# Optimization experiments

Measured on AMD Instinct MI355X. Metric: run time of the kernel, lower is better.

Reference implementation:

```python
import jax, jax.numpy as jnp
import numpy as np

NUM_BINS = 11
SIGMA = 0.1
EMB = 110
FC2 = 512
NUM_CLASSES = 4
DN = ('NCHW', 'OIHW', 'NCHW')


def conv(x, w, b, stride, pad):
    y = jax.lax.conv_general_dilated(x, w, (stride, stride), [(pad, pad), (pad, pad)], dimension_numbers=DN)
    return y + b[None, :, None, None]


def conv_transpose(x, w, b, stride):
    # torch ConvTranspose2d(k=3, padding=1, output_padding=stride-1)
    # == dilated conv with flipped, channel-swapped kernel
    wf = jnp.flip(w, (2, 3)).transpose(1, 0, 2, 3)  # (Cin,Cout,kh,kw)->(Cout,Cin,kh,kw)
    pad = (1, 1 + stride - 1)  # (k-1-p, k-1-p+output_padding)
    y = jax.lax.conv_general_dilated(x, wf, (1, 1), [pad, pad], lhs_dilation=(stride, stride), dimension_numbers=DN)
    return y + b[None, :, None, None]


def kde(data, num_bins, bandwidth):
    # data: (B, N, F) -> (B, F*num_bins), vectorized over features
    pts = jnp.linspace(0.0, 1.0, num_bins, dtype=data.dtype)  # (bins,)
    c = 1.0 / (bandwidth * np.sqrt(2.0 * np.pi))
    coef = -1.0 / (2.0 * bandwidth ** 2)
    diff2 = (pts[None, None, None, :] - data[..., None]) ** 2  # (B,N,F,bins)
    gk = c * jnp.exp(coef * diff2)
    dens = gk.sum(axis=1)  # (B,F,bins) -- integrate over instances
    dens = dens / dens.sum(axis=2, keepdims=True)
    B = data.shape[0]
    return dens.reshape(B, -1)  # feature-major concat, same as torch cat over features


def setup_inputs() -> dict:
    key = jax.random.key(0)
    ks = jax.random.split(key, 16)
    B, N = 64, 32
    g = lambda k, shape, s=0.05: (jax.random.normal(k, shape, dtype=jnp.float32) * s)
    inp = {
        'x': jax.random.uniform(ks[0], (B, N, 3, 32, 32), dtype=jnp.float32),
        'ew1': g(ks[1], (16, 3, 3, 3)), 'eb1': jnp.full((16,), 0.1, jnp.float32),
        'ew2': g(ks[2], (32, 16, 3, 3)), 'eb2': jnp.full((32,), 0.1, jnp.float32),
        'ew3': g(ks[3], (64, 32, 3, 3)), 'eb3': jnp.full((64,), 0.1, jnp.float32),
        'kw': g(ks[4], (EMB, 64 * 8 * 8), 0.02), 'kb': jnp.zeros((EMB,), jnp.float32),
        'dw1': g(ks[5], (64, 64, 3, 3)), 'db1': jnp.zeros((64,), jnp.float32),
        'dw2': g(ks[6], (64, 32, 3, 3)), 'db2': jnp.zeros((32,), jnp.float32),
        'dw3': g(ks[7], (32, 16, 3, 3)), 'db3': jnp.zeros((16,), jnp.float32),
        'dw4': g(ks[8], (3, 16, 1, 1)), 'db4': jnp.full((3,), 0.1, jnp.float32),
        'f1w': g(ks[9], (FC2, EMB * NUM_BINS), 0.02), 'f1b': jnp.zeros((FC2,), jnp.float32),
        'f2w': g(ks[10], (FC2 // 2, FC2), 0.02), 'f2b': jnp.zeros((FC2 // 2,), jnp.float32),
        'f3w': g(ks[11], (NUM_CLASSES, FC2 // 2), 0.02), 'f3b': jnp.zeros((NUM_CLASSES,), jnp.float32),
    }
    return inp


def reference(x, ew1, eb1, ew2, eb2, ew3, eb3, kw, kb,
              dw1, db1, dw2, db2, dw3, db3, dw4, db4,
              f1w, f1b, f2w, f2b, f3w, f3b):
    B, N, C, H, W = x.shape
    xf = x.reshape(B * N, C, H, W)
    # encoder
    h = jax.nn.relu(conv(xf, ew1, eb1, 1, 1))   # (BN,16,32,32)
    h = jax.nn.relu(conv(h, ew2, eb2, 2, 1))    # (BN,32,16,16)
    h = jax.nn.relu(conv(h, ew3, eb3, 2, 1))    # (BN,64,8,8)
    # decoder
    d = jax.nn.relu(conv_transpose(h, dw1, db1, 2))  # (BN,64,16,16)
    d = jax.nn.relu(conv_transpose(d, dw2, db2, 2))  # (BN,32,32,32)
    d = jax.nn.relu(conv_transpose(d, dw3, db3, 1))  # (BN,16,32,32)
    d = conv(d, dw4, db4, 1, 0)                      # (BN,3,32,32)
    decoded_img = d.reshape(B, N, C, H, W)
    # KDE embeddings
    emb = jax.nn.sigmoid(h.reshape(B * N, -1) @ kw.T + kb)  # (BN,EMB)
    emb = emb.reshape(B, N, EMB)
    fd = kde(emb, NUM_BINS, SIGMA)  # (B, EMB*NUM_BINS)
    # MLP classifier (dropout p=0 -> identity)
    m = jax.nn.relu(fd @ f1w.T + f1b)
    m = jax.nn.relu(m @ f2w.T + f2b)
    logits = m @ f3w.T + f3b
    return (logits, decoded_img)
```

## Files before the change

### kernel.cpp

```cpp
#include <hip/hip_runtime.h>
#include <hip/hip_bf16.h>
#include <stdint.h>

typedef __hip_bfloat16 bf16;
typedef __attribute__((ext_vector_type(8))) short short8;
typedef __attribute__((ext_vector_type(4))) float f32x4;

__device__ __forceinline__ bf16 f2b(float v){ return __float2bfloat16(v); }
__device__ __forceinline__ short s2s(float v){ bf16 b = __float2bfloat16(v); return *reinterpret_cast<short*>(&b); }
__device__ __forceinline__ short8 s8zero()
{
    short8 z;
    for (int i = 0; i < 8; ++i) z[i] = 0;
    return z;
}

__global__ void prep_weights(const float* __restrict__ ew1, const float* __restrict__ ew2,
                             const float* __restrict__ ew3, const float* __restrict__ dw1,
                             const float* __restrict__ dw2, const float* __restrict__ dw3,
                             const float* __restrict__ kw,  const float* __restrict__ f1w,
                             const float* __restrict__ f2w,
                             bf16* __restrict__ wte1, bf16* __restrict__ wte2,
                             bf16* __restrict__ wte3, bf16* __restrict__ wtb4,
                             bf16* __restrict__ wtb5, bf16* __restrict__ wtb6,
                             bf16* __restrict__ kwt,  bf16* __restrict__ wtf1,
                             bf16* __restrict__ wtf2)
{
    int idx = blockIdx.x * blockDim.x + threadIdx.x;
    if (idx < 1536) {
        int q = idx >> 9, r = idx & 511;
        int co = r >> 5, k = r & 31;
        int j = k >> 3, ci = k & 7;
        int t = 4 * q + j;
        float v = (ci < 3 && t < 9) ? ew1[((size_t)co * 3 + ci) * 9 + t] : 0.f;
        wte1[idx] = f2b(v);
        return;
    }
    idx -= 1536;
    if (idx < 5120) {
        int p = idx >> 10, r = idx & 1023;
        int co = r >> 5, k = r & 31;
        int t = 2 * p + (k >> 4);
        int ch = k & 15;
        float v = (t <= 8) ? ew2[((size_t)co * 16 + ch) * 9 + t] : 0.f;
        wte2[idx] = f2b(v);
        return;
    }
    idx -= 5120;
    if (idx < 18432) {
        int co = idx / 288;
        int r  = idx - co * 288;
        int ci = r / 9, t = r - ci * 9;
        wte3[((size_t)t * 64 + co) * 32 + ci] = f2b(ew3[idx]);
        return;
    }
    idx -= 18432;
    if (idx < 36864) {
        int ci = idx / 576;
        int r  = idx - ci * 576;
        int co = r / 9, t = r - co * 9;
        wtb4[((size_t)t * 64 + co) * 64 + ci] = f2b(dw1[idx]);
        return;
    }
    idx -= 36864;
    if (idx < 18432) {
        int ci = idx / 288;
        int r  = idx - ci * 288;
        int co = r / 9, t = r - co * 9;
        wtb5[((size_t)t * 32 + co) * 64 + ci] = f2b(dw2[idx]);
        return;
    }
    idx -= 18432;
    if (idx < 4608) {
        int ci = idx / 144;
        int r  = idx - ci * 144;
        int co = r / 9, t = r - co * 9;
        wtb6[((size_t)t * 16 + co) * 32 + ci] = f2b(dw3[idx]);
        return;
    }
    idx -= 4608;
    if (idx < 458752) {
        int e = idx >> 12, kk = idx & 4095;
        int pos = kk >> 6, ci = kk & 63;
        float v = (e < 110) ? kw[(size_t)e * 4096 + ci * 64 + pos] : 0.f;
        kwt[idx] = f2b(v);
        return;
    }
    idx -= 458752;
    if (idx < 655360) {
        int n = idx / 1280, k = idx - n * 1280;
        float v = (k < 1210) ? f1w[(size_t)n * 1210 + k] : 0.f;
        wtf1[idx] = f2b(v);
        return;
    }
    idx -= 655360;
    if (idx < 131072) {
        wtf2[idx] = f2b(f2w[idx]);
        return;
    }
}

__global__ __launch_bounds__(256)
void enc123_fused(const float* __restrict__ xg,
                  const bf16* __restrict__ wte1, const float* __restrict__ eb1,
                  const bf16* __restrict__ wte2, const float* __restrict__ eb2,
                  const bf16* __restrict__ wte3, const float* __restrict__ eb3,
                  bf16* __restrict__ h3g)
{
    __shared__ char smem[57728];
    short8* H1  = (short8*)smem;
    short8* Xs1 = (short8*)(smem + 36992);
    short8* H2  = (short8*)(smem + 36992);

    const int img = blockIdx.x;
    const int tid = threadIdx.x;
    const float* xi = xg + (size_t)img * 3072;

    for (int e = tid; e < 1156; e += 256) {
        int hr = e / 34, wc = e % 34;
        int hi = hr - 1, wi = wc - 1;
        short8 v = s8zero();
        if ((unsigned)hi < 32u && (unsigned)wi < 32u) {
            int p = hi * 32 + wi;
            v[0] = s2s(xi[p]);
            v[1] = s2s(xi[p + 1024]);
            v[2] = s2s(xi[p + 2048]);
        }
        Xs1[e] = v;
    }
    for (int e = tid; e < 264; e += 256) {
        int c8 = e & 1, q = e >> 1;
        int pl = q / 33, j = q % 33;
        int pos = (j < 17) ? j : (j - 16) * 17;
        H1[(pl * 289 + pos) * 2 + c8] = s8zero();
    }
    __syncthreads();

    const int wv = tid >> 6, lane = tid & 63;
    const int lp = lane & 15, lq = lane >> 4;

    {
        short8 wf[3];
        #pragma unroll
        for (int q = 0; q < 3; ++q)
            wf[q] = *reinterpret_cast<const short8*>(wte1 + (size_t)(q * 16 + lp) * 32 + lq * 8);
        float bv[4];
        #pragma unroll
        for (int r = 0; r < 4; ++r) bv[r] = eb1[lq * 4 + r];

        for (int mt = wv * 16; mt < wv * 16 + 16; ++mt) {
            int m = mt * 16 + lp;
            int ho = m >> 5, wo = m & 31;
            f32x4 acc = {0.f, 0.f, 0.f, 0.f};
            #pragma unroll
            for (int q = 0; q < 3; ++q) {
                int t = 4 * q + lq;
                if (t > 8) t = 8;
                int pos = (ho + t / 3) * 34 + (wo + t % 3);
                acc = __builtin_amdgcn_mfma_f32_16x16x32_bf16(wf[q], Xs1[pos], acc, 0, 0, 0);
            }
            int pl  = (ho & 1) * 2 + (wo & 1);
            int pos = ((ho >> 1) + 1) * 17 + ((wo >> 1) + 1);
            int slot = (pl * 289 + pos) * 2 + ((lq >> 1) ^ (pos & 1));
            __align__(8) bf16 ov[4];
            #pragma unroll
            for (int r = 0; r < 4; ++r) ov[r] = f2b(fmaxf(acc[r] + bv[r], 0.f));
            *reinterpret_cast<uint2*>(reinterpret_cast<char*>(&H1[slot]) + (lq & 1) * 8)
                = *reinterpret_cast<uint2*>(ov);
        }
    }
    __syncthreads();

    for (int e = tid; e < 272; e += 256) {
        int c8 = e & 3, q = e >> 2;
        int pl = q / 17, j = q % 17;
        int pos = (j < 9) ? j : (j - 8) * 9;
        H2[(pl * 81 + pos) * 4 + c8] = s8zero();
    }
    {
        const int nt = wv & 1, mh = wv >> 1;
        short8 wf[5];
        #pragma unroll
        for (int p = 0; p < 5; ++p)
            wf[p] = *reinterpret_cast<const short8*>(wte2 + ((size_t)(p * 32 + nt * 16 + lp)) * 32 + lq * 8);
        float bv[4];
        #pragma unroll
        for (int r = 0; r < 4; ++r) bv[r] = eb2[nt * 16 + lq * 4 + r];

        for (int mt = mh * 8; mt < mh * 8 + 8; ++mt) {
            int m = mt * 16 + lp;
            int ho = m >> 4, wo = m & 15;
            f32x4 acc = {0.f, 0.f, 0.f, 0.f};
            #pragma unroll
            for (int p = 0; p < 5; ++p) {
                const int tA = 2 * p, tB = (p < 4) ? 2 * p + 1 : 8;
                const int khA = tA / 3, kwA = tA % 3;
                const int paA = (khA == 1) ? 0 : 1, dhA = (khA == 0) ? -1 : 0;
                const int pbA = (kwA == 1) ? 0 : 1, dwA = (kwA == 0) ? -1 : 0;
                const int khB = tB / 3, kwB = tB % 3;
                const int paB = (khB == 1) ? 0 : 1, dhB = (khB == 0) ? -1 : 0;
                const int pbB = (kwB == 1) ? 0 : 1, dwB = (kwB == 0) ? -1 : 0;
                int posA = (ho + dhA + 1) * 17 + (wo + dwA + 1);
                int posB = (ho + dhB + 1) * 17 + (wo + dwB + 1);
                int idxA = ((paA * 2 + pbA) * 289 + posA) * 2 + ((lq & 1) ^ (posA & 1));
                int idxB = ((paB * 2 + pbB) * 289 + posB) * 2 + ((lq & 1) ^ (posB & 1));
                short8 b = H1[(lq < 2) ? idxA : idxB];
                acc = __builtin_amdgcn_mfma_f32_16x16x32_bf16(wf[p], b, acc, 0, 0, 0);
            }
            int pl  = (ho & 1) * 2 + (wo & 1);
            int pos = ((ho >> 1) + 1) * 9 + ((wo >> 1) + 1);
            int c8w = nt * 2 + (lq >> 1);
            int slot = (pl * 81 + pos) * 4 + (c8w ^ (pos & 3));
            __align__(8) bf16 ov[4];
            #pragma unroll
            for (int r = 0; r < 4; ++r) ov[r] = f2b(fmaxf(acc[r] + bv[r], 0.f));
            *reinterpret_cast<uint2*>(reinterpret_cast<char*>(&H2[slot]) + (lq & 1) * 8)
                = *reinterpret_cast<uint2*>(ov);
        }
    }
    __syncthreads();

    {
        const int nt = wv;
        short8 wf[9];
        #pragma unroll
        for (int t = 0; t < 9; ++t)
            wf[t] = *reinterpret_cast<const short8*>(wte3 + ((size_t)(t * 64 + nt * 16 + lp)) * 32 + lq * 8);
        float bv[4];
        #pragma unroll
        for (int r = 0; r < 4; ++r) bv[r] = eb3[nt * 16 + lq * 4 + r];

        bf16* yi = h3g + (size_t)img * 4096;
        for (int mt = 0; mt < 4; ++mt) {
            int m = mt * 16 + lp;
            int ho = m >> 3, wo = m & 7;
            f32x4 acc = {0.f, 0.f, 0.f, 0.f};
            #pragma unroll
            for (int t = 0; t < 9; ++t) {
                const int kh = t / 3, kw2 = t % 3;
                const int pa = (kh == 1) ? 0 : 1, dh = (kh == 0) ? -1 : 0;
                const int pb = (kw2 == 1) ? 0 : 1, dw = (kw2 == 0) ? -1 : 0;
                int pos = (ho + dh + 1) * 9 + (wo + dw + 1);
                int idx = ((pa * 2 + pb) * 81 + pos) * 4 + (lq ^ (pos & 3));
                acc = __builtin_amdgcn_mfma_f32_16x16x32_bf16(wf[t], H2[idx], acc, 0, 0, 0);
            }
            __align__(8) bf16 ov[4];
            #pragma unroll
            for (int r = 0; r < 4; ++r) ov[r] = f2b(fmaxf(acc[r] + bv[r], 0.f));
            *reinterpret_cast<uint2*>(yi + ((size_t)(ho * 8 + wo)) * 64 + nt * 16 + lq * 4)
                = *reinterpret_cast<uint2*>(ov);
        }
    }
}

__global__ __launch_bounds__(256)
void dec12_fused(const bf16* __restrict__ h3g,
                 const bf16* __restrict__ wtb4, const float* __restrict__ db1,
                 const bf16* __restrict__ wtb5, const float* __restrict__ db2,
                 bf16* __restrict__ d2p)
{
    __shared__ short8 H3s[648];
    __shared__ short8 D1s[2312];
    const int img = blockIdx.x;
    const int tid = threadIdx.x;
    const bf16* xi = h3g + (size_t)img * 4096;

    for (int e = tid; e < 648; e += 256) {
        int c8 = e & 7, pos = e >> 3;
        int hl = pos / 9, wi = pos % 9;
        short8 v = s8zero();
        if (hl < 8 && wi < 8)
            v = *reinterpret_cast<const short8*>(xi + ((size_t)(hl * 8 + wi)) * 64 + c8 * 8);
        H3s[pos * 8 + (c8 ^ (pos & 7))] = v;
    }
    for (int e = tid; e < 264; e += 256) {
        int c8 = e & 7, q = e >> 3;
        int pos = (q < 17) ? (16 * 17 + q) : ((q - 17) * 17 + 16);
        D1s[pos * 8 + c8] = s8zero();
    }
    __syncthreads();

    const int wv = tid >> 6, lane = tid & 63;
    const int lp = lane & 15, lq = lane >> 4;

    {
        const int nt = wv;
        short8 wf[9][2];
        #pragma unroll
        for (int t = 0; t < 9; ++t) {
            const bf16* wp = wtb4 + ((size_t)t * 64 + nt * 16 + lp) * 64 + lq * 8;
            wf[t][0] = *reinterpret_cast<const short8*>(wp);
            wf[t][1] = *reinterpret_cast<const short8*>(wp + 32);
        }
        float bv[4];
        #pragma unroll
        for (int r = 0; r < 4; ++r) bv[r] = db1[nt * 16 + lq * 4 + r];

        const int c8w = nt * 2 + (lq >> 1);
        for (int mt = 0; mt < 4; ++mt) {
            int m = mt * 16 + lp;
            int hq = m >> 3, wq = m & 7;
            f32x4 zero = {0.f, 0.f, 0.f, 0.f};
            f32x4 acc[4] = {zero, zero, zero, zero};
            #pragma unroll
            for (int kh = 0; kh < 3; ++kh) {
                #pragma unroll
                for (int kw = 0; kw < 3; ++kw) {
                    const int pa = (kh + 1) & 1, pb = (kw + 1) & 1;
                    const int oh = (pa + 1 - kh) >> 1, ow = (pb + 1 - kw) >> 1;
                    const int cls = pa * 2 + pb;
                    const int t = kh * 3 + kw;
                    int pos = (hq + oh) * 9 + (wq + ow);
                    int sw = pos & 7;
                    acc[cls] = __builtin_amdgcn_mfma_f32_16x16x32_bf16(wf[t][0], H3s[pos * 8 + (lq ^ sw)], acc[cls], 0, 0, 0);
                    acc[cls] = __builtin_amdgcn_mfma_f32_16x16x32_bf16(wf[t][1], H3s[pos * 8 + ((4 + lq) ^ sw)], acc[cls], 0, 0, 0);
                }
            }
            #pragma unroll
            for (int cls = 0; cls < 4; ++cls) {
                int pa = cls >> 1, pb = cls & 1;
                int ho = hq * 2 + pa, wo = wq * 2 + pb;
                int pos = ho * 17 + wo;
                int slot = pos * 8 + (c8w ^ (pos & 7));
                __align__(8) bf16 ov[4];
                #pragma unroll
                for (int r = 0; r < 4; ++r) ov[r] = f2b(fmaxf(acc[cls][r] + bv[r], 0.f));
                *reinterpret_cast<uint2*>(reinterpret_cast<char*>(&D1s[slot]) + (lq & 1) * 8)
                    = *reinterpret_cast<uint2*>(ov);
            }
        }
    }
    __syncthreads();

    {
        const int nt = wv & 1;
        const int mt0 = (wv >> 1) * 8;
        short8 wf[9][2];
        #pragma unroll
        for (int t = 0; t < 9; ++t) {
            const bf16* wp = wtb5 + ((size_t)t * 32 + nt * 16 + lp) * 64 + lq * 8;
            wf[t][0] = *reinterpret_cast<const short8*>(wp);
            wf[t][1] = *reinterpret_cast<const short8*>(wp + 32);
        }
        float bv[4];
        #pragma unroll
        for (int r = 0; r < 4; ++r) bv[r] = db2[nt * 16 + lq * 4 + r];

        bf16* yo = d2p + (size_t)img * 32768;
        for (int mt = mt0; mt < mt0 + 8; ++mt) {
            const int hq = mt, wq = lp;
            f32x4 zero = {0.f, 0.f, 0.f, 0.f};
            f32x4 acc[4] = {zero, zero, zero, zero};
            #pragma unroll
            for (int kh = 0; kh < 3; ++kh) {
                #pragma unroll
                for (int kw = 0; kw < 3; ++kw) {
                    const int pa = (kh + 1) & 1, pb = (kw + 1) & 1;
                    const int oh = (pa + 1 - kh) >> 1, ow = (pb + 1 - kw) >> 1;
                    const int cls = pa * 2 + pb;
                    const int t = kh * 3 + kw;
                    int pos = (hq + oh) * 17 + (wq + ow);
                    int sw = pos & 7;
                    acc[cls] = __builtin_amdgcn_mfma_f32_16x16x32_bf16(wf[t][0], D1s[pos * 8 + (lq ^ sw)], acc[cls], 0, 0, 0);
                    acc[cls] = __builtin_amdgcn_mfma_f32_16x16x32_bf16(wf[t][1], D1s[pos * 8 + ((4 + lq) ^ sw)], acc[cls], 0, 0, 0);
                }
            }
            #pragma unroll
            for (int cls = 0; cls < 4; ++cls) {
                __align__(8) bf16 ov[4];
                #pragma unroll
                for (int r = 0; r < 4; ++r) ov[r] = f2b(fmaxf(acc[cls][r] + bv[r], 0.f));
                size_t off = (size_t)cls * 8192 + (size_t)nt * 4096 + (hq * 16 + wq) * 16 + lq * 4;
                *reinterpret_cast<uint2*>(yo + off) = *reinterpret_cast<uint2*>(ov);
            }
        }
    }
}

__global__ __launch_bounds__(256)
void emb_mfma(const bf16* __restrict__ h3b, const bf16* __restrict__ kwt,
              const float* __restrict__ kb, float* __restrict__ emb)
{
    __shared__ f32x4 Ls[3][64];
    const int imgbase = blockIdx.x * 16;
    const int nt = blockIdx.y;
    const int w = threadIdx.x >> 6, lane = threadIdx.x & 63;
    const int lp = lane & 15, lq = lane >> 4;
    const int k0 = w * 1024;

    f32x4 acc = {0.f, 0.f, 0.f, 0.f};
    const bf16* bp = h3b + (size_t)(imgbase + lp) * 4096 + k0 + lq * 8;
    const bf16* ap = kwt + (size_t)(nt * 16 + lp) * 4096 + k0 + lq * 8;
    for (int ks = 0; ks < 32; ++ks) {
        short8 bfrag = *reinterpret_cast<const short8*>(bp + ks * 32);
        short8 afrag = *reinterpret_cast<const short8*>(ap + ks * 32);
        acc = __builtin_amdgcn_mfma_f32_16x16x32_bf16(afrag, bfrag, acc, 0, 0, 0);
    }
    if (w > 0) Ls[w - 1][lane] = acc;
    __syncthreads();
    if (w == 0) {
        #pragma unroll
        for (int ww = 0; ww < 3; ++ww) acc += Ls[ww][lane];
        const int e0 = nt * 16 + lq * 4;
        #pragma unroll
        for (int r = 0; r < 4; ++r) {
            int e = e0 + r;
            if (e < 110) {
                float v = acc[r] + kb[e];
                emb[(size_t)(imgbase + lp) * 110 + e] = 1.f / (1.f + expf(-v));
            }
        }
    }
}

__global__ __launch_bounds__(256)
void convt1_mfma_fused(const bf16* __restrict__ d2p, const bf16* __restrict__ wtb,
                       const float* __restrict__ bias,
                       const float* __restrict__ w4, const float* __restrict__ b4,
                       float* __restrict__ dec)
{
    constexpr int C8 = 4;
    constexpr int HR = 18, WR = 34, NPOS = HR * WR;
    __shared__ short8 Xs[NPOS * C8];

    const int img  = blockIdx.x >> 1;
    const int half = blockIdx.x & 1;
    const int hbase = half * 16;
    const bf16* xi = d2p + (size_t)img * 32768;

    for (int e = threadIdx.x; e < NPOS * C8; e += 256) {
        int c8 = e & 3, pos = e >> 2;
        int hr = pos / WR, wr = pos % WR;
        int hi = hbase - 1 + hr, wi = wr - 1;
        short8 v = s8zero();
        if ((unsigned)hi < 32u && (unsigned)wi < 32u) {
            int cls = ((hi & 1) << 1) | (wi & 1);
            size_t src = (size_t)cls * 8192 + (size_t)(c8 >> 1) * 4096
                       + (((hi >> 1) << 4) + (wi >> 1)) * 16 + (c8 & 1) * 8;
            v = *reinterpret_cast<const short8*>(xi + src);
        }
        Xs[pos * C8 + (c8 ^ (pos & 3))] = v;
    }
    __syncthreads();

    const int wv = threadIdx.x >> 6, lane = threadIdx.x & 63;
    const int lp = lane & 15, lq = lane >> 4;

    short8 wf[9];
    #pragma unroll
    for (int t = 0; t < 9; ++t)
        wf[t] = *reinterpret_cast<const short8*>(wtb + ((size_t)t * 16 + lp) * 32 + lq * 8);
    float bv[4];
    #pragma unroll
    for (int r = 0; r < 4; ++r) bv[r] = bias[lq * 4 + r];
    float w4r[3][4];
    #pragma unroll
    for (int j = 0; j < 3; ++j)
        #pragma unroll
        for (int r = 0; r < 4; ++r) w4r[j][r] = w4[j * 16 + lq * 4 + r];
    float b4r[3] = {b4[0], b4[1], b4[2]};

    for (int mt = wv; mt < 32; mt += 4) {
        int m = mt * 16 + lp;
        int hol = m >> 5, wo = m & 31;
        f32x4 acc = {0.f, 0.f, 0.f, 0.f};
        #pragma unroll
        for (int t = 0; t < 9; ++t) {
            int kh = t / 3, kw = t % 3;
            int pos = (hol + 2 - kh) * WR + (wo + 2 - kw);
            short8 b0 = Xs[pos * C8 + (lq ^ (pos & 3))];
            acc = __builtin_amdgcn_mfma_f32_16x16x32_bf16(wf[t], b0, acc, 0, 0, 0);
        }
        float s0 = 0.f, s1 = 0.f, s2 = 0.f;
        #pragma unroll
        for (int r = 0; r < 4; ++r) {
            float v = fmaxf(acc[r] + bv[r], 0.f);
            s0 += v * w4r[0][r]; s1 += v * w4r[1][r]; s2 += v * w4r[2][r];
        }
        s0 += __shfl_xor(s0, 16); s0 += __shfl_xor(s0, 32);
        s1 += __shfl_xor(s1, 16); s1 += __shfl_xor(s1, 32);
        s2 += __shfl_xor(s2, 16); s2 += __shfl_xor(s2, 32);
        if (lq == 0) {
            int ho = hbase + hol;
            size_t base = (size_t)img * 3072 + ho * 32 + wo;
            dec[base]        = s0 + b4r[0];
            dec[base + 1024] = s1 + b4r[1];
            dec[base + 2048] = s2 + b4r[2];
        }
    }
}

__global__ __launch_bounds__(256)
void kde_kernel(const float* __restrict__ emb, bf16* __restrict__ fdb)
{
    __shared__ float es[3520];
    const int b = blockIdx.x, tid = threadIdx.x;
    for (int i = tid; i < 3520; i += 256) es[i] = emb[(size_t)b * 3520 + i];
    __syncthreads();
    if (tid < 110) {
        float dens[11];
        #pragma unroll
        for (int j = 0; j < 11; ++j) dens[j] = 0.f;
        for (int n = 0; n < 32; ++n) {
            float e = es[n * 110 + tid];
            #pragma unroll
            for (int j = 0; j < 11; ++j) {
                float d = 0.1f * j - e;
                dens[j] += __expf(-50.f * d * d);
            }
        }
        float s = 0.f;
        #pragma unroll
        for (int j = 0; j < 11; ++j) s += dens[j];
        float inv = 1.f / s;
        #pragma unroll
        for (int j = 0; j < 11; ++j)
            fdb[(size_t)b * 1280 + tid * 11 + j] = f2b(dens[j] * inv);
    } else if (tid >= 128 && tid < 198) {
        fdb[(size_t)b * 1280 + 1210 + (tid - 128)] = f2b(0.f);
    }
}

template<int K, int N, int RELU>
__global__ __launch_bounds__(256)
void dense_mfma(const bf16* __restrict__ inb, const bf16* __restrict__ wtb,
                const float* __restrict__ bias, bf16* __restrict__ outb)
{
    __shared__ f32x4 Ls[3][64];
    constexpr int KW = K / 4;
    const int mt = blockIdx.x, nt = blockIdx.y;
    const int w = threadIdx.x >> 6, lane = threadIdx.x & 63;
    const int lp = lane & 15, lq = lane >> 4;
    const int k0 = w * KW;

    f32x4 acc = {0.f, 0.f, 0.f, 0.f};
    const bf16* bp = inb + (size_t)(mt * 16 + lp) * K + k0 + lq * 8;
    const bf16* ap = wtb + (size_t)(nt * 16 + lp) * K + k0 + lq * 8;
    for (int ks = 0; ks < KW / 32; ++ks) {
        short8 bfrag = *reinterpret_cast<const short8*>(bp + ks * 32);
        short8 afrag = *reinterpret_cast<const short8*>(ap + ks * 32);
        acc = __builtin_amdgcn_mfma_f32_16x16x32_bf16(afrag, bfrag, acc, 0, 0, 0);
    }
    if (w > 0) Ls[w - 1][lane] = acc;
    __syncthreads();
    if (w == 0) {
        #pragma unroll
        for (int ww = 0; ww < 3; ++ww) acc += Ls[ww][lane];
        const int b = mt * 16 + lp;
        const int o0 = nt * 16 + lq * 4;
        __align__(8) bf16 ov[4];
        #pragma unroll
        for (int r = 0; r < 4; ++r) {
            float v = acc[r] + bias[o0 + r];
            if (RELU) v = fmaxf(v, 0.f);
            ov[r] = f2b(v);
        }
        *reinterpret_cast<uint2*>(outb + (size_t)b * N + o0) = *reinterpret_cast<uint2*>(ov);
    }
}

__global__ __launch_bounds__(256)
void f3_kernel(const bf16* __restrict__ m2b, const float* __restrict__ f3w,
               const float* __restrict__ f3b, float* __restrict__ logits)
{
    __shared__ float m2s[64 * 256];
    const int tid = threadIdx.x;
    for (int i = tid; i < 16384; i += 256) m2s[i] = __bfloat162float(m2b[i]);
    __syncthreads();
    int b = tid >> 2, o = tid & 3;
    float a = f3b[o];
    const float* wr = f3w + o * 256;
    for (int k = 0; k < 256; ++k) a += m2s[b * 256 + k] * wr[k];
    logits[b * 4 + o] = a;
}

extern "C" void kernel_launch(void* const* d_in, const int* in_sizes, int n_in,
                              void* d_out, int out_size, void* d_ws, size_t ws_size,
                              hipStream_t stream)
{
    const float* x    = (const float*)d_in[0];
    const float* ew1  = (const float*)d_in[1];
    const float* eb1  = (const float*)d_in[2];
    const float* ew2  = (const float*)d_in[3];
    const float* eb2  = (const float*)d_in[4];
    const float* ew3  = (const float*)d_in[5];
    const float* eb3  = (const float*)d_in[6];
    const float* kw   = (const float*)d_in[7];
    const float* kb   = (const float*)d_in[8];
    const float* dw1  = (const float*)d_in[9];
    const float* db1  = (const float*)d_in[10];
    const float* dw2  = (const float*)d_in[11];
    const float* db2  = (const float*)d_in[12];
    const float* dw3  = (const float*)d_in[13];
    const float* db3  = (const float*)d_in[14];
    const float* dw4  = (const float*)d_in[15];
    const float* db4  = (const float*)d_in[16];
    const float* f1w  = (const float*)d_in[17];
    const float* f1b  = (const float*)d_in[18];
    const float* f2w  = (const float*)d_in[19];
    const float* f2b_ = (const float*)d_in[20];
    const float* f3w  = (const float*)d_in[21];
    const float* f3b  = (const float*)d_in[22];

    char* ws = (char*)d_ws;
    float* emb  = (float*)(ws + 0);
    bf16*  fdb  = (bf16*) (ws + 901120);
    bf16*  m1b  = (bf16*) (ws + 1064960);
    bf16*  m2b  = (bf16*) (ws + 1130496);
    bf16*  wte1 = (bf16*) (ws + 1163264);
    bf16*  wte2 = (bf16*) (ws + 1166336);
    bf16*  wte3 = (bf16*) (ws + 1176576);
    bf16*  wtb4 = (bf16*) (ws + 1213440);
    bf16*  wtb5 = (bf16*) (ws + 1287168);
    bf16*  wtb6 = (bf16*) (ws + 1324032);
    bf16*  kwt  = (bf16*) (ws + 1333248);
    bf16*  wtf1 = (bf16*) (ws + 2250752);
    bf16*  wtf2 = (bf16*) (ws + 3561472);
    const size_t FIXED = 3823616;

    const size_t PER_IMG = 73728;
    int CHUNK = 2048;
    while (CHUNK > 16 && FIXED + (size_t)CHUNK * PER_IMG > ws_size) CHUNK >>= 1;
    const int NCHUNK = 2048 / CHUNK;

    char* p   = ws + FIXED;
    bf16* h3b = (bf16*)(p);
    bf16* d2p = (bf16*)(p + (size_t)CHUNK * 8192);

    float* logits = (float*)d_out;
    float* dec    = (float*)d_out + 256;

    prep_weights<<<(1330176 + 255)/256, 256, 0, stream>>>(
        ew1, ew2, ew3, dw1, dw2, dw3, kw, f1w, f2w,
        wte1, wte2, wte3, wtb4, wtb5, wtb6, kwt, wtf1, wtf2);

    for (int c = 0; c < NCHUNK; ++c) {
        const float* xc   = x   + (size_t)c * CHUNK * 3 * 1024;
        float*       decc = dec + (size_t)c * CHUNK * 3 * 1024;
        float*       embc = emb + (size_t)c * CHUNK * 110;

        enc123_fused<<<CHUNK, 256, 0, stream>>>(xc, wte1, eb1, wte2, eb2, wte3, eb3, h3b);
        emb_mfma<<<dim3(CHUNK/16, 7), 256, 0, stream>>>(h3b, kwt, kb, embc);
        dec12_fused<<<CHUNK, 256, 0, stream>>>(h3b, wtb4, db1, wtb5, db2, d2p);
        convt1_mfma_fused<<<CHUNK*2, 256, 0, stream>>>(d2p, wtb6, db3, dw4, db4, decc);
    }

    kde_kernel<<<64, 256, 0, stream>>>(emb, fdb);
    dense_mfma<1280, 512, 1><<<dim3(4, 32), 256, 0, stream>>>(fdb, wtf1, f1b, m1b);
    dense_mfma<512, 256, 1> <<<dim3(4, 16), 256, 0, stream>>>(m1b, wtf2, f2b_, m2b);
    f3_kernel<<<1, 256, 0, stream>>>(m2b, f3w, f3b, logits);
}
```

Measured before the change: 213.6 us.

## Fuse final transposed conv and 1x1 conv into decoder kernel via shared memory

Merges the third decoder stage (convT 32->16 plus the 1x1 output conv) into the dec12 kernel. The 32x32x32 bf16 intermediate is kept in LDS instead of going through a global round trip, and one kernel launch per chunk is removed. In exchange each block now needs about 110KB of dynamic shared memory, which limits occupancy to roughly one block per CU. The stage-3 work for each image also runs inside a single 256-thread block instead of being split across two.

```diff
diff --git a/kernel.cpp b/kernel.cpp
--- a/kernel.cpp
+++ b/kernel.cpp
@@ -254,13 +254,18 @@
 }
 
 __global__ __launch_bounds__(256)
-void dec12_fused(const bf16* __restrict__ h3g,
-                 const bf16* __restrict__ wtb4, const float* __restrict__ db1,
-                 const bf16* __restrict__ wtb5, const float* __restrict__ db2,
-                 bf16* __restrict__ d2p)
-{
-    __shared__ short8 H3s[648];
-    __shared__ short8 D1s[2312];
+void dec_fused(const bf16* __restrict__ h3g,
+               const bf16* __restrict__ wtb4, const float* __restrict__ db1,
+               const bf16* __restrict__ wtb5, const float* __restrict__ db2,
+               const bf16* __restrict__ wtb6, const float* __restrict__ db3,
+               const float* __restrict__ w4, const float* __restrict__ b4,
+               float* __restrict__ dec)
+{
+    extern __shared__ char smem[];
+    short8* H3s = (short8*)smem;
+    short8* D1s = (short8*)(smem + 10368);
+    short8* D2s = (short8*)(smem + 47360);
+
     const int img = blockIdx.x;
     const int tid = threadIdx.x;
     const bf16* xi = h3g + (size_t)img * 4096;
@@ -278,6 +283,7 @@
         int pos = (q < 17) ? (16 * 17 + q) : ((q - 17) * 17 + 16);
         D1s[pos * 8 + c8] = s8zero();
     }
+    if (tid == 0) D2s[4096] = s8zero();
     __syncthreads();
 
     const int wv = tid >> 6, lane = tid & 63;
@@ -346,7 +352,7 @@
         #pragma unroll
         for (int r = 0; r < 4; ++r) bv[r] = db2[nt * 16 + lq * 4 + r];
 
-        bf16* yo = d2p + (size_t)img * 32768;
+        const int c8w = nt * 2 + (lq >> 1);
         for (int mt = mt0; mt < mt0 + 8; ++mt) {
             const int hq = mt, wq = lp;
             f32x4 zero = {0.f, 0.f, 0.f, 0.f};
@@ -367,11 +373,63 @@
             }
             #pragma unroll
             for (int cls = 0; cls < 4; ++cls) {
+                int pa = cls >> 1, pb = cls & 1;
+                int p32 = (hq * 2 + pa) * 32 + (wq * 2 + pb);
+                int slot = p32 * 4 + (c8w ^ (p32 & 3));
                 __align__(8) bf16 ov[4];
                 #pragma unroll
                 for (int r = 0; r < 4; ++r) ov[r] = f2b(fmaxf(acc[cls][r] + bv[r], 0.f));
-                size_t off = (size_t)cls * 8192 + (size_t)nt * 4096 + (hq * 16 + wq) * 16 + lq * 4;
-                *reinterpret_cast<uint2*>(yo + off) = *reinterpret_cast<uint2*>(ov);
+                *reinterpret_cast<uint2*>(reinterpret_cast<char*>(&D2s[slot]) + (lq & 1) * 8)
+                    = *reinterpret_cast<uint2*>(ov);
+            }
+        }
+    }
+    __syncthreads();
+
+    {
+        short8 wf[9];
+        #pragma unroll
+        for (int t = 0; t < 9; ++t)
+            wf[t] = *reinterpret_cast<const short8*>(wtb6 + ((size_t)t * 16 + lp) * 32 + lq * 8);
+        float bv[4];
+        #pragma unroll
+        for (int r = 0; r < 4; ++r) bv[r] = db3[lq * 4 + r];
+        float w4r[3][4];
+        #pragma unroll
+        for (int j = 0; j < 3; ++j)
+            #pragma unroll
+            for (int r = 0; r < 4; ++r) w4r[j][r] = w4[j * 16 + lq * 4 + r];
+        float b4r[3] = {b4[0], b4[1], b4[2]};
+
+        for (int mt = wv; mt < 64; mt += 4) {
+            int m = mt * 16 + lp;
+            int ho = m >> 5, wo = m & 31;
+            f32x4 acc = {0.f, 0.f, 0.f, 0.f};
+            #pragma unroll
+            for (int t = 0; t < 9; ++t) {
+                int kh = t / 3, kw = t % 3;
+                int hi = ho + 1 - kh, wi = wo + 1 - kw;
+                int slot = 4096;
+                if ((unsigned)hi < 32u && (unsigned)wi < 32u) {
+                    int p32 = hi * 32 + wi;
+                    slot = p32 * 4 + (lq ^ (p32 & 3));
+                }
+                acc = __builtin_amdgcn_mfma_f32_16x16x32_bf16(wf[t], D2s[slot], acc, 0, 0, 0);
+            }
+            float s0 = 0.f, s1 = 0.f, s2 = 0.f;
+            #pragma unroll
+            for (int r = 0; r < 4; ++r) {
+                float v = fmaxf(acc[r] + bv[r], 0.f);
+                s0 += v * w4r[0][r]; s1 += v * w4r[1][r]; s2 += v * w4r[2][r];
+            }
+            s0 += __shfl_xor(s0, 16); s0 += __shfl_xor(s0, 32);
+            s1 += __shfl_xor(s1, 16); s1 += __shfl_xor(s1, 32);
+            s2 += __shfl_xor(s2, 16); s2 += __shfl_xor(s2, 32);
+            if (lq == 0) {
+                size_t base = (size_t)img * 3072 + ho * 32 + wo;
+                dec[base]        = s0 + b4r[0];
+                dec[base + 1024] = s1 + b4r[1];
+                dec[base + 2048] = s2 + b4r[2];
             }
         }
     }
@@ -409,83 +467,6 @@
                 float v = acc[r] + kb[e];
                 emb[(size_t)(imgbase + lp) * 110 + e] = 1.f / (1.f + expf(-v));
             }
-        }
-    }
-}
-
-__global__ __launch_bounds__(256)
-void convt1_mfma_fused(const bf16* __restrict__ d2p, const bf16* __restrict__ wtb,
-                       const float* __restrict__ bias,
-                       const float* __restrict__ w4, const float* __restrict__ b4,
-                       float* __restrict__ dec)
-{
-    constexpr int C8 = 4;
-    constexpr int HR = 18, WR = 34, NPOS = HR * WR;
-    __shared__ short8 Xs[NPOS * C8];
-
-    const int img  = blockIdx.x >> 1;
-    const int half = blockIdx.x & 1;
-    const int hbase = half * 16;
-    const bf16* xi = d2p + (size_t)img * 32768;
-
-    for (int e = threadIdx.x; e < NPOS * C8; e += 256) {
-        int c8 = e & 3, pos = e >> 2;
-        int hr = pos / WR, wr = pos % WR;
-        int hi = hbase - 1 + hr, wi = wr - 1;
-        short8 v = s8zero();
-        if ((unsigned)hi < 32u && (unsigned)wi < 32u) {
-            int cls = ((hi & 1) << 1) | (wi & 1);
-            size_t src = (size_t)cls * 8192 + (size_t)(c8 >> 1) * 4096
-                       + (((hi >> 1) << 4) + (wi >> 1)) * 16 + (c8 & 1) * 8;
-            v = *reinterpret_cast<const short8*>(xi + src);
-        }
-        Xs[pos * C8 + (c8 ^ (pos & 3))] = v;
-    }
-    __syncthreads();
-
-    const int wv = threadIdx.x >> 6, lane = threadIdx.x & 63;
-    const int lp = lane & 15, lq = lane >> 4;
-
-    short8 wf[9];
-    #pragma unroll
-    for (int t = 0; t < 9; ++t)
-        wf[t] = *reinterpret_cast<const short8*>(wtb + ((size_t)t * 16 + lp) * 32 + lq * 8);
-    float bv[4];
-    #pragma unroll
-    for (int r = 0; r < 4; ++r) bv[r] = bias[lq * 4 + r];
-    float w4r[3][4];
-    #pragma unroll
-    for (int j = 0; j < 3; ++j)
-        #pragma unroll
-        for (int r = 0; r < 4; ++r) w4r[j][r] = w4[j * 16 + lq * 4 + r];
-    float b4r[3] = {b4[0], b4[1], b4[2]};
-
-    for (int mt = wv; mt < 32; mt += 4) {
-        int m = mt * 16 + lp;
-        int hol = m >> 5, wo = m & 31;
-        f32x4 acc = {0.f, 0.f, 0.f, 0.f};
-        #pragma unroll
-        for (int t = 0; t < 9; ++t) {
-            int kh = t / 3, kw = t % 3;
-            int pos = (hol + 2 - kh) * WR + (wo + 2 - kw);
-            short8 b0 = Xs[pos * C8 + (lq ^ (pos & 3))];
-            acc = __builtin_amdgcn_mfma_f32_16x16x32_bf16(wf[t], b0, acc, 0, 0, 0);
-        }
-        float s0 = 0.f, s1 = 0.f, s2 = 0.f;
-        #pragma unroll
-        for (int r = 0; r < 4; ++r) {
-            float v = fmaxf(acc[r] + bv[r], 0.f);
-            s0 += v * w4r[0][r]; s1 += v * w4r[1][r]; s2 += v * w4r[2][r];
-        }
-        s0 += __shfl_xor(s0, 16); s0 += __shfl_xor(s0, 32);
-        s1 += __shfl_xor(s1, 16); s1 += __shfl_xor(s1, 32);
-        s2 += __shfl_xor(s2, 16); s2 += __shfl_xor(s2, 32);
-        if (lq == 0) {
-            int ho = hbase + hol;
-            size_t base = (size_t)img * 3072 + ho * 32 + wo;
-            dec[base]        = s0 + b4r[0];
-            dec[base + 1024] = s1 + b4r[1];
-            dec[base + 2048] = s2 + b4r[2];
         }
     }
 }
@@ -618,17 +599,18 @@
     bf16*  wtf2 = (bf16*) (ws + 3561472);
     const size_t FIXED = 3823616;
 
-    const size_t PER_IMG = 73728;
+    const size_t PER_IMG = 8192;
     int CHUNK = 2048;
     while (CHUNK > 16 && FIXED + (size_t)CHUNK * PER_IMG > ws_size) CHUNK >>= 1;
     const int NCHUNK = 2048 / CHUNK;
 
-    char* p   = ws + FIXED;
-    bf16* h3b = (bf16*)(p);
-    bf16* d2p = (bf16*)(p + (size_t)CHUNK * 8192);
+    bf16* h3b = (bf16*)(ws + FIXED);
 
     float* logits = (float*)d_out;
     float* dec    = (float*)d_out + 256;
+
+    const int DEC_SMEM = 112912;
+    hipFuncSetAttribute((const void*)dec_fused, hipFuncAttributeMaxDynamicSharedMemorySize, DEC_SMEM);
 
     prep_weights<<<(1330176 + 255)/256, 256, 0, stream>>>(
         ew1, ew2, ew3, dw1, dw2, dw3, kw, f1w, f2w,
@@ -641,8 +623,8 @@
 
         enc123_fused<<<CHUNK, 256, 0, stream>>>(xc, wte1, eb1, wte2, eb2, wte3, eb3, h3b);
         emb_mfma<<<dim3(CHUNK/16, 7), 256, 0, stream>>>(h3b, kwt, kb, embc);
-        dec12_fused<<<CHUNK, 256, 0, stream>>>(h3b, wtb4, db1, wtb5, db2, d2p);
-        convt1_mfma_fused<<<CHUNK*2, 256, 0, stream>>>(d2p, wtb6, db3, dw4, db4, decc);
+        dec_fused<<<CHUNK, 256, DEC_SMEM, stream>>>(h3b, wtb4, db1, wtb5, db2,
+                                                    wtb6, db3, dw4, db4, decc);
     }
 
     kde_kernel<<<64, 256, 0, stream>>>(emb, fdb);
```

New measurement: 251.8 us. 1.18x slower.

## Split fused decoder stages into two row-halves per image

Applied to the files above, without the earlier changes.

The fused convtranspose1+2 kernel now launches two blocks per image, each handling half of the output rows with a halo row of the intermediate. This halves shared memory per block and doubles the grid to raise occupancy and parallelism. In exchange, the first stage recomputes one overlapping halo row in the first half, and some MFMA tiles are partly masked.

```diff
diff --git a/kernel.cpp b/kernel.cpp
--- a/kernel.cpp
+++ b/kernel.cpp
@@ -254,30 +254,31 @@
 }
 
 __global__ __launch_bounds__(256)
-void dec12_fused(const bf16* __restrict__ h3g,
-                 const bf16* __restrict__ wtb4, const float* __restrict__ db1,
-                 const bf16* __restrict__ wtb5, const float* __restrict__ db2,
-                 bf16* __restrict__ d2p)
-{
-    __shared__ short8 H3s[648];
-    __shared__ short8 D1s[2312];
-    const int img = blockIdx.x;
-    const int tid = threadIdx.x;
+void dec12_half(const bf16* __restrict__ h3g,
+                const bf16* __restrict__ wtb4, const float* __restrict__ db1,
+                const bf16* __restrict__ wtb5, const float* __restrict__ db2,
+                bf16* __restrict__ d2p)
+{
+    __shared__ short8 H3s[6 * 9 * 8];
+    __shared__ short8 D1s[9 * 17 * 8];
+
+    const int img  = blockIdx.x >> 1;
+    const int half = blockIdx.x & 1;
+    const int h0   = half * 8;
+    const int r3b  = half * 4;
+    const int tid  = threadIdx.x;
     const bf16* xi = h3g + (size_t)img * 4096;
 
-    for (int e = tid; e < 648; e += 256) {
+    for (int e = tid; e < 432; e += 256) {
         int c8 = e & 7, pos = e >> 3;
-        int hl = pos / 9, wi = pos % 9;
+        int lr = pos / 9, wc = pos % 9;
+        int gr = r3b + lr;
         short8 v = s8zero();
-        if (hl < 8 && wi < 8)
-            v = *reinterpret_cast<const short8*>(xi + ((size_t)(hl * 8 + wi)) * 64 + c8 * 8);
+        if (gr < 8 && wc < 8)
+            v = *reinterpret_cast<const short8*>(xi + ((size_t)(gr * 8 + wc)) * 64 + c8 * 8);
         H3s[pos * 8 + (c8 ^ (pos & 7))] = v;
     }
-    for (int e = tid; e < 264; e += 256) {
-        int c8 = e & 7, q = e >> 3;
-        int pos = (q < 17) ? (16 * 17 + q) : ((q - 17) * 17 + 16);
-        D1s[pos * 8 + c8] = s8zero();
-    }
+    for (int e = tid; e < 1224; e += 256) D1s[e] = s8zero();
     __syncthreads();
 
     const int wv = tid >> 6, lane = tid & 63;
@@ -285,6 +286,8 @@
 
     {
         const int nt = wv;
+        const int NQ = (half == 0) ? 5 : 4;
+        const int NPOS = NQ * 8;
         short8 wf[9][2];
         #pragma unroll
         for (int t = 0; t < 9; ++t) {
@@ -297,9 +300,12 @@
         for (int r = 0; r < 4; ++r) bv[r] = db1[nt * 16 + lq * 4 + r];
 
         const int c8w = nt * 2 + (lq >> 1);
-        for (int mt = 0; mt < 4; ++mt) {
-            int m = mt * 16 + lp;
-            int hq = m >> 3, wq = m & 7;
+        const int NPT = (NPOS + 15) / 16;
+        for (int pt = 0; pt < NPT; ++pt) {
+            int m = pt * 16 + lp;
+            bool mvalid = m < NPOS;
+            int mm = mvalid ? m : 0;
+            int lr3 = mm >> 3, wq3 = mm & 7;
             f32x4 zero = {0.f, 0.f, 0.f, 0.f};
             f32x4 acc[4] = {zero, zero, zero, zero};
             #pragma unroll
@@ -310,7 +316,7 @@
                     const int oh = (pa + 1 - kh) >> 1, ow = (pb + 1 - kw) >> 1;
                     const int cls = pa * 2 + pb;
                     const int t = kh * 3 + kw;
-                    int pos = (hq + oh) * 9 + (wq + ow);
+                    int pos = (lr3 + oh) * 9 + (wq3 + ow);
                     int sw = pos & 7;
                     acc[cls] = __builtin_amdgcn_mfma_f32_16x16x32_bf16(wf[t][0], H3s[pos * 8 + (lq ^ sw)], acc[cls], 0, 0, 0);
                     acc[cls] = __builtin_amdgcn_mfma_f32_16x16x32_bf16(wf[t][1], H3s[pos * 8 + ((4 + lq) ^ sw)], acc[cls], 0, 0, 0);
@@ -319,14 +325,17 @@
             #pragma unroll
             for (int cls = 0; cls < 4; ++cls) {
                 int pa = cls >> 1, pb = cls & 1;
-                int ho = hq * 2 + pa, wo = wq * 2 + pb;
-                int pos = ho * 17 + wo;
-                int slot = pos * 8 + (c8w ^ (pos & 7));
-                __align__(8) bf16 ov[4];
-                #pragma unroll
-                for (int r = 0; r < 4; ++r) ov[r] = f2b(fmaxf(acc[cls][r] + bv[r], 0.f));
-                *reinterpret_cast<uint2*>(reinterpret_cast<char*>(&D1s[slot]) + (lq & 1) * 8)
-                    = *reinterpret_cast<uint2*>(ov);
+                int ld = lr3 * 2 + pa;
+                int wo = wq3 * 2 + pb;
+                if (mvalid && ld <= 8) {
+                    int pos = ld * 17 + wo;
+                    int slot = pos * 8 + (c8w ^ (pos & 7));
+                    __align__(8) bf16 ov[4];
+                    #pragma unroll
+                    for (int r = 0; r < 4; ++r) ov[r] = f2b(fmaxf(acc[cls][r] + bv[r], 0.f));
+                    *reinterpret_cast<uint2*>(reinterpret_cast<char*>(&D1s[slot]) + (lq & 1) * 8)
+                        = *reinterpret_cast<uint2*>(ov);
+                }
             }
         }
     }
@@ -334,7 +343,7 @@
 
     {
         const int nt = wv & 1;
-        const int mt0 = (wv >> 1) * 8;
+        const int mt0 = (wv >> 1) * 4;
         short8 wf[9][2];
         #pragma unroll
         for (int t = 0; t < 9; ++t) {
@@ -347,8 +356,8 @@
         for (int r = 0; r < 4; ++r) bv[r] = db2[nt * 16 + lq * 4 + r];
 
         bf16* yo = d2p + (size_t)img * 32768;
-        for (int mt = mt0; mt < mt0 + 8; ++mt) {
-            const int hq = mt, wq = lp;
+        for (int mt = mt0; mt < mt0 + 4; ++mt) {
+            const int hql = mt, wq = lp;
             f32x4 zero = {0.f, 0.f, 0.f, 0.f};
             f32x4 acc[4] = {zero, zero, zero, zero};
             #pragma unroll
@@ -359,18 +368,19 @@
                     const int oh = (pa + 1 - kh) >> 1, ow = (pb + 1 - kw) >> 1;
                     const int cls = pa * 2 + pb;
                     const int t = kh * 3 + kw;
-                    int pos = (hq + oh) * 17 + (wq + ow);
+                    int pos = (hql + oh) * 17 + (wq + ow);
                     int sw = pos & 7;
                     acc[cls] = __builtin_amdgcn_mfma_f32_16x16x32_bf16(wf[t][0], D1s[pos * 8 + (lq ^ sw)], acc[cls], 0, 0, 0);
                     acc[cls] = __builtin_amdgcn_mfma_f32_16x16x32_bf16(wf[t][1], D1s[pos * 8 + ((4 + lq) ^ sw)], acc[cls], 0, 0, 0);
                 }
             }
+            const int hqg = h0 + hql;
             #pragma unroll
             for (int cls = 0; cls < 4; ++cls) {
                 __align__(8) bf16 ov[4];
                 #pragma unroll
                 for (int r = 0; r < 4; ++r) ov[r] = f2b(fmaxf(acc[cls][r] + bv[r], 0.f));
-                size_t off = (size_t)cls * 8192 + (size_t)nt * 4096 + (hq * 16 + wq) * 16 + lq * 4;
+                size_t off = (size_t)cls * 8192 + (size_t)nt * 4096 + (hqg * 16 + wq) * 16 + lq * 4;
                 *reinterpret_cast<uint2*>(yo + off) = *reinterpret_cast<uint2*>(ov);
             }
         }
@@ -641,7 +651,7 @@
 
         enc123_fused<<<CHUNK, 256, 0, stream>>>(xc, wte1, eb1, wte2, eb2, wte3, eb3, h3b);
         emb_mfma<<<dim3(CHUNK/16, 7), 256, 0, stream>>>(h3b, kwt, kb, embc);
-        dec12_fused<<<CHUNK, 256, 0, stream>>>(h3b, wtb4, db1, wtb5, db2, d2p);
+        dec12_half<<<CHUNK*2, 256, 0, stream>>>(h3b, wtb4, db1, wtb5, db2, d2p);
         convt1_mfma_fused<<<CHUNK*2, 256, 0, stream>>>(d2p, wtb6, db3, dw4, db4, decc);
     }
 
```

After: 238.9 us. +11.8%, slower.
